# Performance work log

Measured on AMD Instinct MI355X. Metric: run time of the kernel, lower is better.

## Reference

```python
import jax, jax.numpy as jnp
import numpy as np

DIM = 256
HALF = DIM // 2
B, S = 32, 4096
U_MAX = 4096          # upper bound on number of unique tree positions (positions < S)
MAX_DEPTH = 13        # bitlen(S) covers all path lengths for positions <= S


def setup_inputs() -> dict:
    key = jax.random.key(0)
    k1, k2, k3, k4, k5 = jax.random.split(key, 5)
    token_types = jax.random.randint(k1, (B, S), 0, 5, dtype=jnp.int32)
    node_positions = jax.random.randint(k2, (B, S), 0, S, dtype=jnp.int32)
    small_vals = jax.random.randint(k3, (B, S), 0, 4, dtype=jnp.int32)
    # deBruijn tokens (type 4) reference tree positions -> values must lie in unique(node_positions)
    token_values = jnp.where(token_types == 4, node_positions,
                   jnp.where(token_types == 3, -1, small_vals)).astype(jnp.int32)
    primitives = jax.random.normal(k4, (2, HALF, HALF), dtype=jnp.float32)
    identity = jnp.ones((1, HALF), dtype=jnp.float32)
    embed_weight = jax.random.normal(k5, (11, HALF), dtype=jnp.float32)
    return {"token_types": token_types, "token_values": token_values,
            "node_positions": node_positions, "primitives": primitives,
            "identity": identity, "embed_weight": embed_weight}


def cayley(X):
    # torch orthogonal(..., orthogonal_map='cayley'): A = tril(X) - tril(X)^T (skew), Q = (I - A/2)^{-1}(I + A/2)
    A = jnp.tril(X)
    A = A - jnp.swapaxes(A, -1, -2)
    I = jnp.eye(X.shape[-1], dtype=X.dtype)
    return jnp.linalg.solve(I - 0.5 * A, I + 0.5 * A)


def _forward(token_types, token_values, node_positions, primitives, identity, embed_weight):
    Q = cayley(primitives)                                   # [2, h, h] orthogonal maps
    flat_pos = node_positions.ravel()
    uniq, inv = jnp.unique(flat_pos, return_inverse=True, size=U_MAX, fill_value=S)
    inv = inv.ravel()

    # binary path of pos: bit d of pos for d < bitlen(pos)-1, padded with 2 (pos<=1 -> empty path)
    d = jnp.arange(MAX_DEPTH, dtype=uniq.dtype)
    bits = (uniq[:, None] >> d) & 1                           # [U, D]
    valid = (uniq[:, None] >> (d + 1)) > 0
    word = jnp.where(valid, bits, 2)                          # [U, D]

    maps0 = jnp.broadcast_to(identity, (U_MAX, HALF)).astype(primitives.dtype)

    def step(maps, b):                                        # maps [U, h], b [U]
        m0 = maps @ Q[0].T                                    # linear(maps, primitives[0])
        m1 = maps @ Q[1].T
        maps = jnp.where((b == 0)[:, None], m0,
                jnp.where((b == 1)[:, None], m1, maps))
        return maps, None

    path_emb, _ = jax.lax.scan(step, maps0, word.T)           # [U, h]

    pos_enc = path_emb[inv].reshape(B, S, HALF)               # positional encodings

    sos = token_types == 0
    bop = token_types == 1
    nop = token_types == 2
    oos = (token_types == 3) & (token_values == -1)
    db = token_types == 4

    emb_idx = jnp.where(bop, token_values + 1,
              jnp.where(nop, token_values + 5, 0))
    type_emb = embed_weight[emb_idx]                          # [B, S, h]

    db_idx = jnp.searchsorted(uniq, jnp.clip(token_values, 0, S - 1))  # bucketize into unique positions
    db_emb = path_emb[db_idx]                                 # [B, S, h]

    content = jnp.zeros_like(pos_enc)
    content = jnp.where(sos[..., None], embed_weight[0], content)
    content = jnp.where((bop | nop)[..., None], type_emb, content)
    content = jnp.where(db[..., None], db_emb, content)
    content = jnp.where(oos[..., None], embed_weight[10], content)

    return jnp.concatenate([content, pos_enc], axis=-1)       # [B, S, DIM]


def reference(token_types, token_values, node_positions, primitives, identity, embed_weight):
    return _forward(token_types, token_values, node_positions, primitives, identity, embed_weight)
```

## Files before the change

kernel.cpp:

```cpp
#include <hip/hip_runtime.h>

#define HALF 128
#define NMAT 16384
#define NTOK 131072

typedef float f4 __attribute__((ext_vector_type(4)));

__global__ __launch_bounds__(512) void cayley_qt(const float* __restrict__ prim,
                                                 float* __restrict__ QT) {
    __shared__ __align__(16) float Xs[128 * 129];
    __shared__ __align__(16) float CpT[2][16][132];
    __shared__ __align__(16) float Rp [2][16][128];
    __shared__ __align__(16) float Dcol[2][16][20];

    const int b = blockIdx.x;
    const float* __restrict__ X = prim + b * NMAT;
    const int t  = threadIdx.x;
    const int c  = t & 127;
    const int q  = t >> 7;
    const int r0 = q << 5;

    for (int idx4 = t; idx4 < 4096; idx4 += 512) {
        int gi = idx4 << 2;
        float4 v = *(const float4*)(X + gi);
        int r = gi >> 7, cc = gi & 127;
        float* p = &Xs[r * 129 + cc];
        p[0] = v.x; p[1] = v.y; p[2] = v.z; p[3] = v.w;
    }
    __syncthreads();

    float reg[32];
    #pragma unroll
    for (int i = 0; i < 32; ++i) {
        int r  = r0 + i;
        int mx = r > c ? r : c;
        int mn = r ^ c ^ mx;
        float x = Xs[mx * 129 + mn];
        reg[i] = (r == c) ? 1.0f : (r > c ? 0.5f * x : -0.5f * x);
    }

    #pragma unroll
    for (int s = 0; s < 8; ++s) {
        const int  p     = s & 1;
        const int  k0    = s << 4;
        const int  q0    = s >> 1;
        const int  kl    = (s & 1) << 4;
        const bool panel = (c >= k0) && (c < k0 + 16);

        if (panel) {
            const int m = c - k0;
            #pragma unroll
            for (int i = 0; i < 32; i += 4)
                *(float4*)&CpT[p][m][r0 + i] =
                    make_float4(reg[i], reg[i+1], reg[i+2], reg[i+3]);
        }
        if (q == q0) {
            #pragma unroll
            for (int j = 0; j < 16; ++j) Rp[p][j][c] = reg[kl + j];
        }
        __syncthreads();

        if (t < 64) {
            const int cp = t & 15, q4 = t >> 4;
            float dd[4];
            #pragma unroll
            for (int i = 0; i < 4; ++i) dd[i] = Rp[p][q4 * 4 + i][k0 + cp];
            #pragma unroll
            for (int k = 0; k < 16; ++k) {
                float cv[4];
                #pragma unroll
                for (int i = 0; i < 4; ++i) cv[i] = __shfl(dd[i], (q4 << 4) | k);
                float rv   = __shfl(dd[k & 3], ((k >> 2) << 4) | cp);
                float dkk  = __shfl(rv, k);
                float dinv = 1.0f / dkk;
                float sv   = rv * dinv;
                bool  own  = (cp == k);
                float rf   = own ? dinv : sv;
                #pragma unroll
                for (int i = 0; i < 4; ++i)
                    dd[i] = own ? (-dd[i] * dinv) : fmaf(-cv[i], sv, dd[i]);
                dd[k & 3] = (q4 == (k >> 2)) ? rf : dd[k & 3];
            }
            #pragma unroll
            for (int i = 0; i < 4; ++i) Dcol[p][cp][q4 * 4 + i] = dd[i];
        }
        __syncthreads();

        float coeff[16];
        if (!panel) {
            #pragma unroll
            for (int j = 0; j < 16; ++j) coeff[j] = 0.0f;
            #pragma unroll
            for (int j = 0; j < 16; ++j) {
                float rpj = Rp[p][j][c];
                #pragma unroll
                for (int mq = 0; mq < 16; mq += 4) {
                    float4 dv = *(const float4*)&Dcol[p][j][mq];
                    coeff[mq+0] = fmaf(dv.x, rpj, coeff[mq+0]);
                    coeff[mq+1] = fmaf(dv.y, rpj, coeff[mq+1]);
                    coeff[mq+2] = fmaf(dv.z, rpj, coeff[mq+2]);
                    coeff[mq+3] = fmaf(dv.w, rpj, coeff[mq+3]);
                }
            }
        } else {
            const int mp = c - k0;
            #pragma unroll
            for (int j = 0; j < 16; ++j) coeff[j] = Dcol[p][mp][j];
            #pragma unroll
            for (int i = 0; i < 32; ++i) reg[i] = 0.0f;
        }

        #pragma unroll
        for (int m = 0; m < 16; ++m) {
            float cm = coeff[m];
            #pragma unroll
            for (int i = 0; i < 32; i += 4) {
                float4 c4 = *(const float4*)&CpT[p][m][r0 + i];
                reg[i+0] = fmaf(-c4.x, cm, reg[i+0]);
                reg[i+1] = fmaf(-c4.y, cm, reg[i+1]);
                reg[i+2] = fmaf(-c4.z, cm, reg[i+2]);
                reg[i+3] = fmaf(-c4.w, cm, reg[i+3]);
            }
        }
        if (q == q0) {
            #pragma unroll
            for (int j = 0; j < 16; ++j) reg[kl + j] = coeff[j];
        }
    }

    float* __restrict__ out = QT + b * NMAT;
    #pragma unroll
    for (int i = 0; i < 32; ++i) {
        int r = r0 + i;
        out[r * HALF + c] = 2.0f * reg[i] - (r == c ? 1.0f : 0.0f);
    }
}

__global__ __launch_bounds__(256) void path_base(const float* __restrict__ QT,
                                                 const float* __restrict__ ident,
                                                 float* __restrict__ P) {
    __shared__ __align__(16) float vs[2][4][HALF];
    const int t    = threadIdx.x;
    const int rg   = t >> 6;
    const int jj   = (t & 63) << 1;
    const int v    = (blockIdx.x << 2) + rg;
    const int vmax = (blockIdx.x << 2) + 3;

    float2 cv = *(const float2*)&ident[jj];
    *(float2*)&vs[0][rg][jj] = cv;
    __syncthreads();

    int cur = 0;
    for (int d = 0; d < 8; ++d) {
        if ((vmax >> (d + 1)) == 0) break;
        const bool valid = (v >> (d + 1)) > 0;
        const float* __restrict__ Qm = QT + (((v >> d) & 1) ? NMAT : 0);
        float2 acc = make_float2(0.f, 0.f);
        #pragma unroll 4
        for (int cc = 0; cc < 128; cc += 4) {
            float4 v4 = *(const float4*)&vs[cur][rg][cc];
            float2 q0 = *(const float2*)&Qm[(cc+0)*HALF + jj];
            float2 q1 = *(const float2*)&Qm[(cc+1)*HALF + jj];
            float2 q2 = *(const float2*)&Qm[(cc+2)*HALF + jj];
            float2 q3 = *(const float2*)&Qm[(cc+3)*HALF + jj];
            acc.x = fmaf(v4.x,q0.x, fmaf(v4.y,q1.x, fmaf(v4.z,q2.x, fmaf(v4.w,q3.x, acc.x))));
            acc.y = fmaf(v4.x,q0.y, fmaf(v4.y,q1.y, fmaf(v4.z,q2.y, fmaf(v4.w,q3.y, acc.y))));
        }
        if (valid) cv = acc;
        *(float2*)&vs[cur ^ 1][rg][jj] = cv;
        __syncthreads();
        cur ^= 1;
    }
    *(float2*)&P[v * HALF + jj] = cv;
}

__global__ __launch_bounds__(256) void path_upper(const float* __restrict__ QT,
                                                  float* __restrict__ P) {
    __shared__ __align__(16) float Qs[128 * 128];
    __shared__ __align__(16) float vs[8][HALF];
    const int t  = threadIdx.x;
    const int rg = t >> 5;
    const int jj = (t & 31) << 2;
    const int k  = 2 + (blockIdx.x >> 4);
    const int r  = ((blockIdx.x & 15) << 3) + rg;
    const int v  = (k << 7) | r;

    float4 cv = *(const float4*)&P[(128 + r) * HALF + jj];

    for (int d = 7; d < 13; ++d) {
        if ((k >> (d - 6)) == 0) break;
        const float* __restrict__ Qm = QT + (((k >> (d - 7)) & 1) ? NMAT : 0);
        *(float4*)&vs[rg][jj] = cv;
        __syncthreads();
        for (int i = t; i < 4096; i += 256)
            *(float4*)&Qs[i << 2] = *(const float4*)&Qm[i << 2];
        __syncthreads();

        float4 acc = make_float4(0.f, 0.f, 0.f, 0.f);
        #pragma unroll 4
        for (int cc = 0; cc < 128; cc += 4) {
            float4 v4 = *(const float4*)&vs[rg][cc];
            float4 q0 = *(const float4*)&Qs[(cc+0)*HALF + jj];
            float4 q1 = *(const float4*)&Qs[(cc+1)*HALF + jj];
            float4 q2 = *(const float4*)&Qs[(cc+2)*HALF + jj];
            float4 q3 = *(const float4*)&Qs[(cc+3)*HALF + jj];
            acc.x = fmaf(v4.x,q0.x, fmaf(v4.y,q1.x, fmaf(v4.z,q2.x, fmaf(v4.w,q3.x, acc.x))));
            acc.y = fmaf(v4.x,q0.y, fmaf(v4.y,q1.y, fmaf(v4.z,q2.y, fmaf(v4.w,q3.y, acc.y))));
            acc.z = fmaf(v4.x,q0.z, fmaf(v4.y,q1.z, fmaf(v4.z,q2.z, fmaf(v4.w,q3.z, acc.z))));
            acc.w = fmaf(v4.x,q0.w, fmaf(v4.y,q1.w, fmaf(v4.z,q2.w, fmaf(v4.w,q3.w, acc.w))));
        }
        cv = acc;
    }
    *(float4*)&P[v * HALF + jj] = cv;
}

__global__ __launch_bounds__(256) void emit_out(const int* __restrict__ tt,
                                                const int* __restrict__ tv,
                                                const int* __restrict__ np,
                                                const float* __restrict__ P,
                                                const float* __restrict__ emb,
                                                float* __restrict__ out) {
    const int i  = (blockIdx.x << 2) + (threadIdx.x >> 6);
    const int jj = (threadIdx.x & 63) << 2;
    const int ty = tt[i];
    const int v  = tv[i];
    f4 val;
    if (jj < 128) {
        if (ty == 0)      val = *(const f4*)&emb[jj];
        else if (ty == 1) val = *(const f4*)&emb[(v + 1) * HALF + jj];
        else if (ty == 2) val = *(const f4*)&emb[(v + 5) * HALF + jj];
        else if (ty == 4) {
            int vc = v < 0 ? 0 : (v > 4095 ? 4095 : v);
            val = *(const f4*)&P[vc * HALF + jj];
        } else if (v == -1) val = *(const f4*)&emb[10 * HALF + jj];
        else { f4 z = {0.f, 0.f, 0.f, 0.f}; val = z; }
    } else {
        const int p = np[i];
        val = *(const f4*)&P[p * HALF + (jj - 128)];
    }
    __builtin_nontemporal_store(val, (f4*)&out[i * 256 + jj]);
}

extern "C" void kernel_launch(void* const* d_in, const int* in_sizes, int n_in,
                              void* d_out, int out_size, void* d_ws, size_t ws_size,
                              hipStream_t stream) {
    const int*   token_types = (const int*)  d_in[0];
    const int*   token_vals  = (const int*)  d_in[1];
    const int*   node_pos    = (const int*)  d_in[2];
    const float* prim        = (const float*)d_in[3];
    const float* ident       = (const float*)d_in[4];
    const float* emb         = (const float*)d_in[5];
    float* out = (float*)d_out;

    float* QT = (float*)d_ws;
    float* P  = (float*)((char*)d_ws + 262144);

    cayley_qt  <<<2,   512, 0, stream>>>(prim, QT);
    path_base  <<<64,  256, 0, stream>>>(QT, ident, P);
    path_upper <<<480, 256, 0, stream>>>(QT, P);
    emit_out   <<<NTOK / 4, 256, 0, stream>>>(token_types, token_vals, node_pos,
                                              P, emb, out);
}
```

Measured before the change: 280.0 us.

## Drop LDS staging of Q in path_upper, read Q from global with register row tiling

path_upper no longer copies the full 128x128 Q matrix into shared memory at each depth step. Each thread now owns one output column for four rows and reads Q directly from global or L2. The vector state is double-buffered in shared memory, so only one barrier per step is needed. This removes the 64KB LDS fill and its barrier, which should raise occupancy, but it depends on cache hits for Q reads that are now scalar per column.

```diff
diff --git a/kernel.cpp b/kernel.cpp
--- a/kernel.cpp
+++ b/kernel.cpp
@@ -176,42 +176,50 @@
 
 __global__ __launch_bounds__(256) void path_upper(const float* __restrict__ QT,
                                                   float* __restrict__ P) {
-    __shared__ __align__(16) float Qs[128 * 128];
-    __shared__ __align__(16) float vs[8][HALF];
+    __shared__ __align__(16) float vs[2][8][HALF];
     const int t  = threadIdx.x;
-    const int rg = t >> 5;
-    const int jj = (t & 31) << 2;
+    const int j  = t & 127;
+    const int h  = t >> 7;
     const int k  = 2 + (blockIdx.x >> 4);
-    const int r  = ((blockIdx.x & 15) << 3) + rg;
-    const int v  = (k << 7) | r;
-
-    float4 cv = *(const float4*)&P[(128 + r) * HALF + jj];
-
+    const int r0 = (blockIdx.x & 15) << 3;
+
+    float acc[4];
+    #pragma unroll
+    for (int rr = 0; rr < 4; ++rr)
+        acc[rr] = P[(128 + r0 + h * 4 + rr) * HALF + j];
+
+    int p = 0;
     for (int d = 7; d < 13; ++d) {
         if ((k >> (d - 6)) == 0) break;
         const float* __restrict__ Qm = QT + (((k >> (d - 7)) & 1) ? NMAT : 0);
-        *(float4*)&vs[rg][jj] = cv;
-        __syncthreads();
-        for (int i = t; i < 4096; i += 256)
-            *(float4*)&Qs[i << 2] = *(const float4*)&Qm[i << 2];
-        __syncthreads();
-
-        float4 acc = make_float4(0.f, 0.f, 0.f, 0.f);
+        #pragma unroll
+        for (int rr = 0; rr < 4; ++rr) vs[p][h * 4 + rr][j] = acc[rr];
+        __syncthreads();
+
+        float nacc[4] = {0.f, 0.f, 0.f, 0.f};
         #pragma unroll 4
         for (int cc = 0; cc < 128; cc += 4) {
-            float4 v4 = *(const float4*)&vs[rg][cc];
-            float4 q0 = *(const float4*)&Qs[(cc+0)*HALF + jj];
-            float4 q1 = *(const float4*)&Qs[(cc+1)*HALF + jj];
-            float4 q2 = *(const float4*)&Qs[(cc+2)*HALF + jj];
-            float4 q3 = *(const float4*)&Qs[(cc+3)*HALF + jj];
-            acc.x = fmaf(v4.x,q0.x, fmaf(v4.y,q1.x, fmaf(v4.z,q2.x, fmaf(v4.w,q3.x, acc.x))));
-            acc.y = fmaf(v4.x,q0.y, fmaf(v4.y,q1.y, fmaf(v4.z,q2.y, fmaf(v4.w,q3.y, acc.y))));
-            acc.z = fmaf(v4.x,q0.z, fmaf(v4.y,q1.z, fmaf(v4.z,q2.z, fmaf(v4.w,q3.z, acc.z))));
-            acc.w = fmaf(v4.x,q0.w, fmaf(v4.y,q1.w, fmaf(v4.z,q2.w, fmaf(v4.w,q3.w, acc.w))));
-        }
-        cv = acc;
-    }
-    *(float4*)&P[v * HALF + jj] = cv;
+            float q0 = Qm[(cc + 0) * HALF + j];
+            float q1 = Qm[(cc + 1) * HALF + j];
+            float q2 = Qm[(cc + 2) * HALF + j];
+            float q3 = Qm[(cc + 3) * HALF + j];
+            #pragma unroll
+            for (int rr = 0; rr < 4; ++rr) {
+                float4 v4 = *(const float4*)&vs[p][h * 4 + rr][cc];
+                nacc[rr] = fmaf(v4.x, q0,
+                           fmaf(v4.y, q1,
+                           fmaf(v4.z, q2,
+                           fmaf(v4.w, q3, nacc[rr]))));
+            }
+        }
+        #pragma unroll
+        for (int rr = 0; rr < 4; ++rr) acc[rr] = nacc[rr];
+        p ^= 1;
+    }
+
+    #pragma unroll
+    for (int rr = 0; rr < 4; ++rr)
+        P[((k << 7) | (r0 + h * 4 + rr)) * HALF + j] = acc[rr];
 }
 
 __global__ __launch_bounds__(256) void emit_out(const int* __restrict__ tt,
```

After: 275.7 us. Within noise of the previous version (-1.5%).
